# Kernel optimization log

Hardware: AMD Instinct MI355X
Metric: run time of the kernel (lower is better)

## Reference

```python
import jax, jax.numpy as jnp
import numpy as np

N_NODES = 100000
N_EDGES = 1600000
IN_CH = 64
HID = 64
OUT_CH = 128
EDGE_CH = 3
OBS_RANGE = 0.5
ATK_RANGE = 0.3


def setup_inputs() -> dict:
    key = jax.random.key(0)
    k = jax.random.split(key, 8)
    # node features: first column is an integer node type in {0,1,2}
    node_type = jax.random.randint(k[0], (N_NODES, 1), 0, 3).astype(jnp.float32)
    feats = jax.random.normal(k[1], (N_NODES, IN_CH - 1), dtype=jnp.float32)
    x = jnp.concatenate([node_type, feats], axis=-1)
    edge_index = jax.random.randint(k[2], (2, N_EDGES), 0, N_NODES)
    # edge_attr[:,0] = distance in [0,1)
    edge_attr = jax.random.uniform(k[3], (N_EDGES, EDGE_CH), dtype=jnp.float32)
    s1 = 1.0 / np.sqrt(2 * IN_CH + EDGE_CH)
    s2 = 1.0 / np.sqrt(HID)
    W1 = jax.random.normal(k[4], (2 * IN_CH + EDGE_CH, HID), dtype=jnp.float32) * s1
    b1 = jnp.zeros((HID,), dtype=jnp.float32)
    W2 = jax.random.normal(k[5], (HID, OUT_CH), dtype=jnp.float32) * s2
    b2 = jnp.zeros((OUT_CH,), dtype=jnp.float32)
    return {"x": x, "edge_index": edge_index, "edge_attr": edge_attr,
            "W1": W1, "b1": b1, "W2": W2, "b2": b2}


def reference(x, edge_index, edge_attr, W1, b1, W2, b2):
    src = edge_index[0]  # j (source)
    dst = edge_index[1]  # i (target)
    x_j = x[src]         # [E, IN_CH]
    x_i = x[dst]         # [E, IN_CH]
    h = jnp.concatenate([x_i, x_j, edge_attr], axis=-1)  # [E, 2*IN_CH+3]
    msg = jax.nn.relu(h @ W1 + b1) @ W2 + b2             # [E, OUT_CH]
    dist = edge_attr[:, 0]
    ntype = x_j[:, 0]
    mask = jnp.where(ntype == 0, dist < OBS_RANGE,
                     jnp.where(ntype == 1, dist < ATK_RANGE, True))
    msg = mask[:, None].astype(msg.dtype) * msg
    out = jax.ops.segment_sum(msg, dst, num_segments=x.shape[0])  # [N, OUT_CH]
    return jax.nn.relu(out)
```

## Files before the change

kernel.cpp:

```cpp
#include <hip/hip_runtime.h>

#define N_NODES 100000
#define N_EDGES 1600000
#define IN_CH   64
#define HID_CH  64
#define OUT_CH  128
#define TILE    128
#define N_TILES (N_EDGES / TILE)

typedef __attribute__((ext_vector_type(8))) __bf16    bf16x8;
typedef __attribute__((ext_vector_type(4))) float     f32x4;
typedef __attribute__((ext_vector_type(2))) _Float16  f16x2;
typedef __attribute__((ext_vector_type(8))) _Float16  f16x8;

__device__ __forceinline__ unsigned short f2bf(float f) {
    union { float f; unsigned int i; } c;
    c.f = f;
    unsigned int u = c.i;
    unsigned int r = (u + 0x7FFFu + ((u >> 16) & 1u)) >> 16;
    return (unsigned short)r;
}

__device__ __forceinline__ void atomic_pk_add_f16(unsigned int* addr, f16x2 val) {
    typedef __attribute__((address_space(1))) f16x2 gf16x2;
    __builtin_amdgcn_global_atomic_fadd_v2f16((gf16x2*)(void*)addr, val);
}

__global__ void gnn_prep(const float* __restrict__ xf,
                         unsigned short* __restrict__ xb,
                         unsigned char* __restrict__ ntype,
                         uint4* __restrict__ hz,
                         float4* __restrict__ cz) {
    int i = blockIdx.x * blockDim.x + threadIdx.x;
    if (i < 1600000) {
        float4 v = reinterpret_cast<const float4*>(xf)[i];
        ushort4 o;
        o.x = f2bf(v.x); o.y = f2bf(v.y); o.z = f2bf(v.z); o.w = f2bf(v.w);
        reinterpret_cast<ushort4*>(xb)[i] = o;
        if ((i & 15) == 0) {
            int n = i >> 4;
            ntype[n] = (v.x == 0.0f) ? 0 : ((v.x == 1.0f) ? 1 : 2);
        }
    } else if (i < 2400000) {
        hz[i - 1600000] = (uint4){0u, 0u, 0u, 0u};
    } else if (i < 2425000) {
        cz[i - 2400000] = (float4){0.f, 0.f, 0.f, 0.f};
    }
}

__global__ __launch_bounds__(256, 4) void gnn_edge_hidden(
    const unsigned char*  __restrict__ ntype,
    const unsigned short* __restrict__ xb,
    const int*            __restrict__ eidx,
    const float*          __restrict__ ea,
    const float*          __restrict__ W1,
    const float*          __restrict__ b1,
    unsigned int*         __restrict__ hsum,
    float*                __restrict__ cnt)
{
    __shared__ __align__(16) unsigned short W1T[64][136];
    __shared__ float w1tail[4][64];
    __shared__ float eas[128][4];
    __shared__ float masks[128];
    __shared__ int   dsts[128];
    __shared__ int   srcs[128];

    const int tid  = threadIdx.x;
    const int wave = tid >> 6;
    const int lane = tid & 63;
    const int q    = lane >> 4;
    const int m16  = lane & 15;

    for (int idx = tid; idx < 128 * 64; idx += 256) {
        int k = idx >> 6, n = idx & 63;
        W1T[n][k] = f2bf(W1[idx]);
    }
    if (tid < 64) {
        w1tail[0][tid] = W1[128 * 64 + tid];
        w1tail[1][tid] = W1[129 * 64 + tid];
        w1tail[2][tid] = W1[130 * 64 + tid];
        w1tail[3][tid] = b1[tid];
    }

    for (int t = blockIdx.x; t < N_TILES; t += gridDim.x) {
        __syncthreads();
        if (tid < 128) {
            int e = t * TILE + tid;
            int s = eidx[e];
            int d = eidx[N_EDGES + e];
            srcs[tid] = s;
            dsts[tid] = d;
            float a0 = ea[e * 3 + 0];
            float a1 = ea[e * 3 + 1];
            float a2 = ea[e * 3 + 2];
            eas[tid][0] = a0; eas[tid][1] = a1; eas[tid][2] = a2;
            int ntc = ntype[s];
            float mk;
            if (ntc == 0)      mk = (a0 < 0.5f) ? 1.0f : 0.0f;
            else if (ntc == 1) mk = (a0 < 0.3f) ? 1.0f : 0.0f;
            else               mk = 1.0f;
            masks[tid] = mk;
            if (mk != 0.0f) unsafeAtomicAdd(&cnt[d], 1.0f);
        }
        __syncthreads();

        const int ebase = wave * 32;

        f32x4 acc1[2][4];
#pragma unroll
        for (int mt = 0; mt < 2; ++mt) {
            float e0[4], e1[4], e2[4];
#pragma unroll
            for (int r = 0; r < 4; ++r) {
                int el = ebase + mt * 16 + q * 4 + r;
                e0[r] = eas[el][0]; e1[r] = eas[el][1]; e2[r] = eas[el][2];
            }
#pragma unroll
            for (int nt = 0; nt < 4; ++nt) {
                int n = nt * 16 + m16;
                float t0 = w1tail[0][n], t1 = w1tail[1][n];
                float t2 = w1tail[2][n], bb = w1tail[3][n];
#pragma unroll
                for (int r = 0; r < 4; ++r)
                    acc1[mt][nt][r] = bb + e0[r] * t0 + e1[r] * t1 + e2[r] * t2;
            }
        }

#pragma unroll
        for (int kc = 0; kc < 4; ++kc) {
            bf16x8 af[2];
#pragma unroll
            for (int mt = 0; mt < 2; ++mt) {
                int el   = ebase + mt * 16 + m16;
                int node = (kc < 2) ? dsts[el] : srcs[el];
                af[mt] = *reinterpret_cast<const bf16x8*>(
                    xb + (size_t)node * IN_CH + (kc & 1) * 32 + q * 8);
            }
#pragma unroll
            for (int nt = 0; nt < 4; ++nt) {
                bf16x8 bfr = *reinterpret_cast<const bf16x8*>(
                    &W1T[nt * 16 + m16][kc * 32 + q * 8]);
                acc1[0][nt] = __builtin_amdgcn_mfma_f32_16x16x32_bf16(af[0], bfr, acc1[0][nt], 0, 0, 0);
                acc1[1][nt] = __builtin_amdgcn_mfma_f32_16x16x32_bf16(af[1], bfr, acc1[1][nt], 0, 0, 0);
            }
        }

#pragma unroll
        for (int mt = 0; mt < 2; ++mt) {
#pragma unroll
            for (int r = 0; r < 4; ++r) {
                int el = ebase + mt * 16 + q * 4 + r;
                float mk = masks[el];
                if (mk != 0.0f) {
                    unsigned int* hbase = hsum + (size_t)dsts[el] * 32;
                    float v0 = acc1[mt][0][r]; v0 = v0 > 0.f ? v0 : 0.f;
                    float v1 = acc1[mt][1][r]; v1 = v1 > 0.f ? v1 : 0.f;
                    float v2 = acc1[mt][2][r]; v2 = v2 > 0.f ? v2 : 0.f;
                    float v3 = acc1[mt][3][r]; v3 = v3 > 0.f ? v3 : 0.f;
                    if (v0 + v1 > 0.f) {
                        f16x2 p01 = {(_Float16)v0, (_Float16)v1};
                        atomic_pk_add_f16(hbase + m16, p01);
                    }
                    if (v2 + v3 > 0.f) {
                        f16x2 p23 = {(_Float16)v2, (_Float16)v3};
                        atomic_pk_add_f16(hbase + 16 + m16, p23);
                    }
                }
            }
        }
    }
}

__global__ __launch_bounds__(256, 4) void gnn_node_out(
    const _Float16* __restrict__ hsum,
    const float*    __restrict__ cnt,
    const float*    __restrict__ W2,
    const float*    __restrict__ b2,
    float*          __restrict__ out)
{
    __shared__ __align__(16) unsigned short W2T[128][72];
    __shared__ float b2s[128];

    const int tid  = threadIdx.x;
    const int wave = tid >> 6;
    const int lane = tid & 63;
    const int q    = lane >> 4;
    const int m16  = lane & 15;

    for (int idx = tid; idx < 64 * 128; idx += 256) {
        int p = idx >> 7, n = idx & 127;
        int ch = (p >> 1) + 16 * (p & 1) + ((p >= 32) ? 16 : 0);
        W2T[n][p] = f2bf(W2[ch * 128 + n]);
    }
    if (tid < 128) b2s[tid] = b2[tid];
    __syncthreads();

    const int nodeBase = (blockIdx.x * 4 + wave) * 32;
    if (nodeBase >= N_NODES) return;

    f32x4 acc[2][8];
#pragma unroll
    for (int mt = 0; mt < 2; ++mt)
#pragma unroll
        for (int nt = 0; nt < 8; ++nt)
            acc[mt][nt] = (f32x4){0.0f, 0.0f, 0.0f, 0.0f};

#pragma unroll
    for (int kc = 0; kc < 2; ++kc) {
        bf16x8 af[2];
#pragma unroll
        for (int mt = 0; mt < 2; ++mt) {
            int node = nodeBase + mt * 16 + m16;
            if (node >= N_NODES) node = N_NODES - 1;
            f16x8 h = *reinterpret_cast<const f16x8*>(
                hsum + (size_t)node * HID_CH + kc * 32 + q * 8);
            union { bf16x8 v; unsigned short u[8]; } rr;
#pragma unroll
            for (int j = 0; j < 8; ++j) rr.u[j] = f2bf((float)h[j]);
            af[mt] = rr.v;
        }
#pragma unroll
        for (int nt = 0; nt < 8; ++nt) {
            bf16x8 bfr = *reinterpret_cast<const bf16x8*>(
                &W2T[nt * 16 + m16][kc * 32 + q * 8]);
            acc[0][nt] = __builtin_amdgcn_mfma_f32_16x16x32_bf16(af[0], bfr, acc[0][nt], 0, 0, 0);
            acc[1][nt] = __builtin_amdgcn_mfma_f32_16x16x32_bf16(af[1], bfr, acc[1][nt], 0, 0, 0);
        }
    }

#pragma unroll
    for (int mt = 0; mt < 2; ++mt) {
        float cc[4]; int nn[4];
#pragma unroll
        for (int r = 0; r < 4; ++r) {
            nn[r] = nodeBase + mt * 16 + q * 4 + r;
            cc[r] = (nn[r] < N_NODES) ? cnt[nn[r]] : 0.0f;
        }
#pragma unroll
        for (int nt = 0; nt < 8; ++nt) {
            int col = nt * 16 + m16;
            float bb = b2s[col];
#pragma unroll
            for (int r = 0; r < 4; ++r) {
                if (nn[r] < N_NODES) {
                    float v = acc[mt][nt][r] + cc[r] * bb;
                    out[(size_t)nn[r] * OUT_CH + col] = v > 0.0f ? v : 0.0f;
                }
            }
        }
    }
}

extern "C" void kernel_launch(void* const* d_in, const int* in_sizes, int n_in,
                              void* d_out, int out_size, void* d_ws, size_t ws_size,
                              hipStream_t stream) {
    const float* x  = (const float*)d_in[0];
    const int*   ei = (const int*)d_in[1];
    const float* ea = (const float*)d_in[2];
    const float* W1 = (const float*)d_in[3];
    const float* b1 = (const float*)d_in[4];
    const float* W2 = (const float*)d_in[5];
    const float* b2 = (const float*)d_in[6];
    float* out = (float*)d_out;

    char* wsb = (char*)d_ws;
    unsigned int*   hsum  = (unsigned int*)wsb;
    float*          cnt   = (float*)(wsb + 12800000);
    unsigned short* xb    = (unsigned short*)(wsb + 13200000);
    unsigned char*  ntype = (unsigned char*)(wsb + 26000000);

    gnn_prep<<<(2425000 + 255) / 256, 256, 0, stream>>>(
        x, xb, ntype, (uint4*)hsum, (float4*)cnt);

    gnn_edge_hidden<<<1792, 256, 0, stream>>>(ntype, xb, ei, ea, W1, b1, hsum, cnt);

    gnn_node_out<<<(N_NODES + 127) / 128, 256, 0, stream>>>(
        (const _Float16*)hsum, cnt, W2, b2, out);
}
```

Measured before the change: 280.8 us.

## Double-buffer edge tile metadata to prefetch next tile during MFMA compute

Edge indices, attributes and node type for the next tile are loaded into registers at the start of each iteration and written to a second shared-memory buffer after the current tile's compute and atomics. This replaces two __syncthreads per tile with one custom lgkmcnt-wait plus s_barrier, hiding global load latency behind compute. Launch bounds rise to 6 blocks per SM and the grid drops to 1536 blocks. The cost is more live registers and more LDS, and the hand-written barrier only waits on lgkmcnt, which relies on the staging loads having already been consumed before the shared stores.

```diff
diff --git a/kernel.cpp b/kernel.cpp
--- a/kernel.cpp
+++ b/kernel.cpp
@@ -13,6 +13,8 @@
 typedef __attribute__((ext_vector_type(2))) _Float16  f16x2;
 typedef __attribute__((ext_vector_type(8))) _Float16  f16x8;
 
+#define LGKM_BARRIER() asm volatile("s_waitcnt lgkmcnt(0)\n\ts_barrier" ::: "memory")
+
 __device__ __forceinline__ unsigned short f2bf(float f) {
     union { float f; unsigned int i; } c;
     c.f = f;
@@ -24,6 +26,12 @@
 __device__ __forceinline__ void atomic_pk_add_f16(unsigned int* addr, f16x2 val) {
     typedef __attribute__((address_space(1))) f16x2 gf16x2;
     __builtin_amdgcn_global_atomic_fadd_v2f16((gf16x2*)(void*)addr, val);
+}
+
+__device__ __forceinline__ float mask_of(int ntc, float a0) {
+    if (ntc == 0) return (a0 < 0.5f) ? 1.0f : 0.0f;
+    if (ntc == 1) return (a0 < 0.3f) ? 1.0f : 0.0f;
+    return 1.0f;
 }
 
 __global__ void gnn_prep(const float* __restrict__ xf,
@@ -48,7 +56,7 @@
     }
 }
 
-__global__ __launch_bounds__(256, 4) void gnn_edge_hidden(
+__global__ __launch_bounds__(256, 6) void gnn_edge_hidden(
     const unsigned char*  __restrict__ ntype,
     const unsigned short* __restrict__ xb,
     const int*            __restrict__ eidx,
@@ -60,10 +68,10 @@
 {
     __shared__ __align__(16) unsigned short W1T[64][136];
     __shared__ float w1tail[4][64];
-    __shared__ float eas[128][4];
-    __shared__ float masks[128];
-    __shared__ int   dsts[128];
-    __shared__ int   srcs[128];
+    __shared__ float eas[2][128][4];
+    __shared__ float masks[2][128];
+    __shared__ int   dsts[2][128];
+    __shared__ int   srcs[2][128];
 
     const int tid  = threadIdx.x;
     const int wave = tid >> 6;
@@ -82,27 +90,41 @@
         w1tail[3][tid] = b1[tid];
     }
 
-    for (int t = blockIdx.x; t < N_TILES; t += gridDim.x) {
-        __syncthreads();
-        if (tid < 128) {
-            int e = t * TILE + tid;
-            int s = eidx[e];
-            int d = eidx[N_EDGES + e];
-            srcs[tid] = s;
-            dsts[tid] = d;
-            float a0 = ea[e * 3 + 0];
-            float a1 = ea[e * 3 + 1];
-            float a2 = ea[e * 3 + 2];
-            eas[tid][0] = a0; eas[tid][1] = a1; eas[tid][2] = a2;
-            int ntc = ntype[s];
-            float mk;
-            if (ntc == 0)      mk = (a0 < 0.5f) ? 1.0f : 0.0f;
-            else if (ntc == 1) mk = (a0 < 0.3f) ? 1.0f : 0.0f;
-            else               mk = 1.0f;
-            masks[tid] = mk;
-            if (mk != 0.0f) unsafeAtomicAdd(&cnt[d], 1.0f);
-        }
-        __syncthreads();
+    const int stride = gridDim.x;
+    int t = blockIdx.x;
+
+    if (tid < 128) {
+        int e = t * TILE + tid;
+        int s = eidx[e];
+        int d = eidx[N_EDGES + e];
+        float a0 = ea[e * 3 + 0];
+        float a1 = ea[e * 3 + 1];
+        float a2 = ea[e * 3 + 2];
+        int ntc = ntype[s];
+        srcs[0][tid] = s; dsts[0][tid] = d;
+        eas[0][tid][0] = a0; eas[0][tid][1] = a1; eas[0][tid][2] = a2;
+        float mk = mask_of(ntc, a0);
+        masks[0][tid] = mk;
+        if (mk != 0.0f) unsafeAtomicAdd(&cnt[d], 1.0f);
+    }
+    LGKM_BARRIER();
+
+    int p = 0;
+    while (t < N_TILES) {
+        const int tn = t + stride;
+        const bool doStage = (tn < N_TILES) && (tid < 128);
+
+        int sN = 0, dN = 0, ntN = 2;
+        float a0N = 0.f, a1N = 0.f, a2N = 0.f;
+        if (doStage) {
+            int e = tn * TILE + tid;
+            sN  = eidx[e];
+            dN  = eidx[N_EDGES + e];
+            a0N = ea[e * 3 + 0];
+            a1N = ea[e * 3 + 1];
+            a2N = ea[e * 3 + 2];
+            ntN = ntype[sN];
+        }
 
         const int ebase = wave * 32;
 
@@ -113,7 +135,7 @@
 #pragma unroll
             for (int r = 0; r < 4; ++r) {
                 int el = ebase + mt * 16 + q * 4 + r;
-                e0[r] = eas[el][0]; e1[r] = eas[el][1]; e2[r] = eas[el][2];
+                e0[r] = eas[p][el][0]; e1[r] = eas[p][el][1]; e2[r] = eas[p][el][2];
             }
 #pragma unroll
             for (int nt = 0; nt < 4; ++nt) {
@@ -132,7 +154,7 @@
 #pragma unroll
             for (int mt = 0; mt < 2; ++mt) {
                 int el   = ebase + mt * 16 + m16;
-                int node = (kc < 2) ? dsts[el] : srcs[el];
+                int node = (kc < 2) ? dsts[p][el] : srcs[p][el];
                 af[mt] = *reinterpret_cast<const bf16x8*>(
                     xb + (size_t)node * IN_CH + (kc & 1) * 32 + q * 8);
             }
@@ -150,9 +172,9 @@
 #pragma unroll
             for (int r = 0; r < 4; ++r) {
                 int el = ebase + mt * 16 + q * 4 + r;
-                float mk = masks[el];
+                float mk = masks[p][el];
                 if (mk != 0.0f) {
-                    unsigned int* hbase = hsum + (size_t)dsts[el] * 32;
+                    unsigned int* hbase = hsum + (size_t)dsts[p][el] * 32;
                     float v0 = acc1[mt][0][r]; v0 = v0 > 0.f ? v0 : 0.f;
                     float v1 = acc1[mt][1][r]; v1 = v1 > 0.f ? v1 : 0.f;
                     float v2 = acc1[mt][2][r]; v2 = v2 > 0.f ? v2 : 0.f;
@@ -168,6 +190,17 @@
                 }
             }
         }
+
+        if (doStage) {
+            srcs[p ^ 1][tid] = sN; dsts[p ^ 1][tid] = dN;
+            eas[p ^ 1][tid][0] = a0N; eas[p ^ 1][tid][1] = a1N; eas[p ^ 1][tid][2] = a2N;
+            float mk = mask_of(ntN, a0N);
+            masks[p ^ 1][tid] = mk;
+            if (mk != 0.0f) unsafeAtomicAdd(&cnt[dN], 1.0f);
+        }
+        LGKM_BARRIER();
+        p ^= 1;
+        t = tn;
     }
 }
 
@@ -272,7 +305,7 @@
     gnn_prep<<<(2425000 + 255) / 256, 256, 0, stream>>>(
         x, xb, ntype, (uint4*)hsum, (float4*)cnt);
 
-    gnn_edge_hidden<<<1792, 256, 0, stream>>>(ntype, xb, ei, ea, W1, b1, hsum, cnt);
+    gnn_edge_hidden<<<1536, 256, 0, stream>>>(ntype, xb, ei, ea, W1, b1, hsum, cnt);
 
     gnn_node_out<<<(N_NODES + 127) / 128, 256, 0, stream>>>(
         (const _Float16*)hsum, cnt, W2, b2, out);
```

After: 313.6 us. 1.12x slower.
